# Optimization experiments

Hardware: AMD Instinct MI355X
Metric: run time of the kernel (lower is better)

## Reference

```python
import jax, jax.numpy as jnp
import numpy as np

MIN_K = 1024  # hard-negative mining floor per image (per_image=True branch)


def setup_inputs() -> dict:
    key = jax.random.key(0)
    k1, k2 = jax.random.split(key)
    B, C, D, H, W = 4, 3, 64, 256, 256
    inp = jax.random.normal(k1, (B, C, D, H, W), dtype=jnp.float32)
    tgt = jax.random.randint(k2, (B, D, H, W), 0, C, dtype=jnp.int64)
    return {"input": inp, "target": tgt}


def reference(input, target):
    b = input.shape[0]
    # per-pixel cross-entropy: -log_softmax over class dim, gathered at target
    logp = jax.nn.log_softmax(input, axis=1)                      # [B,C,D,H,W]
    ce = -jnp.take_along_axis(logp, target[:, None].astype(jnp.int32), axis=1)[:, 0]
    loss = ce.reshape(b, -1)                                      # [B, N]
    tflat = target.reshape(b, -1)                                 # [B, N]
    N = loss.shape[1]

    fg = tflat > 0                                                # [B, N]
    fg_num = fg.sum(axis=1)                                       # [B] int
    bg_num = N - fg_num                                           # [B] int
    k = jnp.minimum(bg_num, jnp.maximum(fg_num, MIN_K))           # [B] int

    # foreground term: mean of fg losses (0 if no fg)
    fg_sum = jnp.where(fg, loss, 0.0).sum(axis=1)                 # [B]
    fg_term = jnp.where(fg_num > 0,
                        fg_sum / jnp.maximum(fg_num, 1).astype(loss.dtype), 0.0)

    # background term: mean of top-k hardest bg losses (data-dependent k, fixed shapes)
    bg_masked = jnp.where(fg, -jnp.inf, loss)                     # fg -> -inf, never selected
    sorted_desc = -jnp.sort(-bg_masked, axis=1)                   # [B, N] descending
    sel = jnp.arange(N)[None, :] < k[:, None]                     # first k entries
    bg_sum = jnp.where(sel, sorted_desc, 0.0).sum(axis=1)         # [B]
    bg_term = jnp.where(bg_num > 0,
                        bg_sum / jnp.maximum(k, 1).astype(loss.dtype), 0.0)

    return jnp.sum(fg_term + bg_term) / b
```

## Files before the change

### kernel.cpp

```cpp
#include <hip/hip_runtime.h>

#define NPIX 4194304
#define BATCH 4
#define MINK 1024ULL
#define NBINS 4096
#define G1 512
#define HG 256

typedef unsigned long long u64;
typedef int vint4 __attribute__((ext_vector_type(4)));
typedef float vflt4 __attribute__((ext_vector_type(4)));

__device__ __forceinline__ float pix_loss(float v0, float v1, float v2, int t) {
    float m = fmaxf(fmaxf(v0, v1), v2);
    float lse = m + __logf(__expf(v0 - m) + __expf(v1 - m) + __expf(v2 - m));
    float xt = (t == 0) ? v0 : ((t == 1) ? v1 : v2);
    return lse - xt;
}

__global__ __launch_bounds__(256) void k_reduce(const float* __restrict__ x,
                                                const int* __restrict__ tg,
                                                float* __restrict__ pfs,
                                                float* __restrict__ pbs,
                                                unsigned* __restrict__ pfc,
                                                uint4* __restrict__ histz,
                                                unsigned* __restrict__ flags,
                                                int have_hist) {
    const int b = blockIdx.y;
    if (b == 0 && blockIdx.x < 32) {
        if (have_hist) histz[blockIdx.x * 256 + threadIdx.x] = make_uint4(0u, 0u, 0u, 0u);
        if (blockIdx.x == 0 && threadIdx.x == 0) flags[1] = 0u;
    }
    const float* xb = x + (size_t)b * 3 * NPIX;
    const int* tb = tg + (size_t)b * NPIX;
    float fs = 0.f, bs = 0.f;
    int fc = 0;
    const int stride = G1 * 256 * 4;
#pragma unroll
    for (int it = 0; it < NPIX / stride; ++it) {
        const int i = it * stride + (blockIdx.x * 256 + threadIdx.x) * 4;
        const vflt4 a = __builtin_nontemporal_load((const vflt4*)(xb + i));
        const vflt4 c = __builtin_nontemporal_load((const vflt4*)(xb + NPIX + i));
        const vflt4 d = __builtin_nontemporal_load((const vflt4*)(xb + 2 * NPIX + i));
        const vint4 t4 = __builtin_nontemporal_load((const vint4*)(tb + i));
        float l;
        l = pix_loss(a[0], c[0], d[0], t4[0]); if (t4[0] > 0) { fs += l; fc++; } else bs += l;
        l = pix_loss(a[1], c[1], d[1], t4[1]); if (t4[1] > 0) { fs += l; fc++; } else bs += l;
        l = pix_loss(a[2], c[2], d[2], t4[2]); if (t4[2] > 0) { fs += l; fc++; } else bs += l;
        l = pix_loss(a[3], c[3], d[3], t4[3]); if (t4[3] > 0) { fs += l; fc++; } else bs += l;
    }
#pragma unroll
    for (int off = 32; off > 0; off >>= 1) {
        fs += __shfl_down(fs, off);
        bs += __shfl_down(bs, off);
        fc += __shfl_down(fc, off);
    }
    __shared__ float sfs[4], sbs[4];
    __shared__ int sfc[4];
    const int wid = threadIdx.x >> 6;
    if ((threadIdx.x & 63) == 0) { sfs[wid] = fs; sbs[wid] = bs; sfc[wid] = fc; }
    __syncthreads();
    if (threadIdx.x == 0) {
        const int slot = b * G1 + blockIdx.x;
        pfs[slot] = sfs[0] + sfs[1] + sfs[2] + sfs[3];
        pbs[slot] = sbs[0] + sbs[1] + sbs[2] + sbs[3];
        pfc[slot] = (unsigned)(sfc[0] + sfc[1] + sfc[2] + sfc[3]);
    }
}

__device__ __forceinline__ void reduce_image(const float* __restrict__ pfs,
                                             const float* __restrict__ pbs,
                                             const unsigned* __restrict__ pfc,
                                             int b2, int tid,
                                             double* __restrict__ sda,
                                             double* __restrict__ sdb,
                                             unsigned* __restrict__ su,
                                             double& tfs, double& tbs, u64& tfc) {
    double fs = 0.0, bs = 0.0;
    unsigned fc = 0;
    if (tid < G1 / 4) {
        const float4 f4 = ((const float4*)pfs)[b2 * (G1 / 4) + tid];
        const float4 b4 = ((const float4*)pbs)[b2 * (G1 / 4) + tid];
        const uint4 c4 = ((const uint4*)pfc)[b2 * (G1 / 4) + tid];
        fs = (double)f4.x + (double)f4.y + (double)f4.z + (double)f4.w;
        bs = (double)b4.x + (double)b4.y + (double)b4.z + (double)b4.w;
        fc = c4.x + c4.y + c4.z + c4.w;
    }
#pragma unroll
    for (int off = 32; off > 0; off >>= 1) {
        fs += __shfl_down(fs, off);
        bs += __shfl_down(bs, off);
        fc += __shfl_down(fc, off);
    }
    const int wid = tid >> 6;
    if ((tid & 63) == 0) { sda[wid] = fs; sdb[wid] = bs; su[wid] = fc; }
    __syncthreads();
    tfs = sda[0] + sda[1] + sda[2] + sda[3];
    tbs = sdb[0] + sdb[1] + sdb[2] + sdb[3];
    tfc = (u64)su[0] + su[1] + su[2] + su[3];
    __syncthreads();
}

__global__ __launch_bounds__(256) void k_tail(const float* __restrict__ pfs,
                                              const float* __restrict__ pbs,
                                              const unsigned* __restrict__ pfc,
                                              const float* __restrict__ x,
                                              const int* __restrict__ tg,
                                              unsigned* __restrict__ hist_cnt,
                                              float* __restrict__ hist_sum,
                                              unsigned* __restrict__ flags,
                                              float* __restrict__ out,
                                              int have_hist) {
    const int b = blockIdx.y;
    const int tid = threadIdx.x;
    __shared__ double sda[4], sdb[4];
    __shared__ unsigned su[4];

    u64 fc_own;
    {
        unsigned s = 0;
        if (tid < G1 / 4) {
            const uint4 c4 = ((const uint4*)pfc)[b * (G1 / 4) + tid];
            s = c4.x + c4.y + c4.z + c4.w;
        }
#pragma unroll
        for (int off = 32; off > 0; off >>= 1) s += __shfl_down(s, off);
        if ((tid & 63) == 0) su[tid >> 6] = s;
        __syncthreads();
        fc_own = (u64)su[0] + su[1] + su[2] + su[3];
        __syncthreads();
    }
    const u64 bg_own = (u64)NPIX - fc_own;
    const u64 mk_own = fc_own > MINK ? fc_own : MINK;
    const u64 k_own = bg_own < mk_own ? bg_own : mk_own;
    const bool need_own = (k_own < bg_own) && have_hist;

    if (blockIdx.x == 0 && b == 0) {
        double acc = 0.0;
        bool any_need = false;
        for (int b2 = 0; b2 < BATCH; ++b2) {
            double tfs, tbs; u64 tfc;
            reduce_image(pfs, pbs, pfc, b2, tid, sda, sdb, su, tfs, tbs, tfc);
            const u64 bg = (u64)NPIX - tfc;
            const u64 mk = tfc > MINK ? tfc : MINK;
            const u64 k = bg < mk ? bg : mk;
            if (k < bg && have_hist) any_need = true;
            const double fg_term = (tfc > 0) ? tfs / (double)tfc : 0.0;
            const u64 kd = k > 1 ? k : 1;
            const double bg_term = (bg > 0) ? tbs / (double)kd : 0.0;
            acc += fg_term + bg_term;
        }
        if (tid == 0 && !any_need) out[0] = (float)(acc / (double)BATCH);
    }

    if (!need_own) return;

    __shared__ unsigned hc[NBINS];
    __shared__ float hs[NBINS];
    for (int i = tid; i < NBINS; i += 256) { hc[i] = 0u; hs[i] = 0.f; }
    __syncthreads();
    {
        const float* xb = x + (size_t)b * 3 * NPIX;
        const int* tb = tg + (size_t)b * NPIX;
        const int stride = HG * 256 * 4;
        for (int i = (blockIdx.x * 256 + tid) * 4; i < NPIX; i += stride) {
            const float4 a = *(const float4*)(xb + i);
            const float4 c = *(const float4*)(xb + NPIX + i);
            const float4 d = *(const float4*)(xb + 2 * NPIX + i);
            const int4 t4 = *(const int4*)(tb + i);
            float v[4][3] = {{a.x, c.x, d.x}, {a.y, c.y, d.y}, {a.z, c.z, d.z}, {a.w, c.w, d.w}};
            int tt[4] = {t4.x, t4.y, t4.z, t4.w};
#pragma unroll
            for (int j = 0; j < 4; ++j) {
                if (tt[j] == 0) {
                    float l = fmaxf(pix_loss(v[j][0], v[j][1], v[j][2], tt[j]), 0.f);
                    unsigned bin = __float_as_uint(l) >> 20;
                    atomicAdd(&hc[bin], 1u);
                    atomicAdd(&hs[bin], l);
                }
            }
        }
    }
    __syncthreads();
    for (int i = tid; i < NBINS; i += 256) {
        if (hc[i]) {
            atomicAdd(&hist_cnt[(size_t)b * NBINS + i], hc[i]);
            atomicAdd(&hist_sum[(size_t)b * NBINS + i], hs[i]);
        }
    }

    int nneed = 0;
    for (int b2 = 0; b2 < BATCH; ++b2) {
        unsigned s = 0;
        if (tid < G1 / 4) {
            const uint4 c4 = ((const uint4*)pfc)[b2 * (G1 / 4) + tid];
            s = c4.x + c4.y + c4.z + c4.w;
        }
#pragma unroll
        for (int off = 32; off > 0; off >>= 1) s += __shfl_down(s, off);
        if ((tid & 63) == 0) su[tid >> 6] = s;
        __syncthreads();
        const u64 fc2 = (u64)su[0] + su[1] + su[2] + su[3];
        __syncthreads();
        const u64 bg2 = (u64)NPIX - fc2;
        const u64 mk2 = fc2 > MINK ? fc2 : MINK;
        const u64 k2 = bg2 < mk2 ? bg2 : mk2;
        if (k2 < bg2) nneed++;
    }

    __threadfence();
    __syncthreads();
    __shared__ int is_last;
    if (tid == 0) {
        unsigned v = atomicAdd(&flags[1], 1u);
        is_last = (v == (unsigned)(HG * nneed) - 1u) ? 1 : 0;
    }
    __syncthreads();
    if (!is_last) return;
    __threadfence();

    double acc = 0.0;
    for (int b2 = 0; b2 < BATCH; ++b2) {
        double tfs, tbs; u64 tfc;
        reduce_image(pfs, pbs, pfc, b2, tid, sda, sdb, su, tfs, tbs, tfc);
        const u64 bg = (u64)NPIX - tfc;
        const u64 mk = tfc > MINK ? tfc : MINK;
        const u64 k = bg < mk ? bg : mk;
        double bg_sel = tbs;
        if (k < bg) {
            for (int i = tid; i < NBINS; i += 256) {
                hc[i] = __hip_atomic_load(&hist_cnt[(size_t)b2 * NBINS + i],
                                          __ATOMIC_ACQUIRE, __HIP_MEMORY_SCOPE_AGENT);
                hs[i] = __hip_atomic_load(&hist_sum[(size_t)b2 * NBINS + i],
                                          __ATOMIC_ACQUIRE, __HIP_MEMORY_SCOPE_AGENT);
            }
            __syncthreads();
            if (tid == 0) {
                u64 cnt = 0; double s = 0.0, topk = 0.0;
                for (int i = NBINS - 1; i >= 0; --i) {
                    unsigned c = hc[i];
                    if (cnt + c >= k) {
                        double edge = (double)__uint_as_float(((unsigned)i) << 20);
                        topk = s + (double)(k - cnt) * edge;
                        break;
                    }
                    cnt += c;
                    s += (double)hs[i];
                }
                sda[0] = topk;
            }
            __syncthreads();
            bg_sel = sda[0];
            __syncthreads();
        }
        const double fg_term = (tfc > 0) ? tfs / (double)tfc : 0.0;
        const u64 kd = k > 1 ? k : 1;
        const double bg_term = (bg > 0) ? bg_sel / (double)kd : 0.0;
        acc += fg_term + bg_term;
    }
    if (tid == 0) out[0] = (float)(acc / (double)BATCH);
}

extern "C" void kernel_launch(void* const* d_in, const int* in_sizes, int n_in,
                              void* d_out, int out_size, void* d_ws, size_t ws_size,
                              hipStream_t stream) {
    const float* x = (const float*)d_in[0];
    const int* tg = (const int*)d_in[1];
    float* out = (float*)d_out;

    char* ws = (char*)d_ws;
    float* pfs = (float*)ws;
    float* pbs = (float*)(ws + 16384);
    unsigned* pfc = (unsigned*)(ws + 32768);
    unsigned* flags = (unsigned*)(ws + 49152);
    unsigned* hist_cnt = (unsigned*)(ws + 49280);
    float* hist_sum = (float*)(ws + 49280 + (size_t)BATCH * NBINS * 4);
    uint4* histz = (uint4*)(ws + 49280);
    const size_t need_ws = 49280 + (size_t)BATCH * NBINS * 8;
    const int have_hist = (ws_size >= need_ws) ? 1 : 0;

    dim3 block(256);
    dim3 grid1(G1, BATCH);
    k_reduce<<<grid1, block, 0, stream>>>(x, tg, pfs, pbs, pfc, histz, flags, have_hist);
    dim3 grid2(HG, BATCH);
    k_tail<<<grid2, block, 0, stream>>>(pfs, pbs, pfc, x, tg,
                                        hist_cnt, hist_sum, flags, out, have_hist);
}
```

Before: 50.81 us.

## Finalize loss in last reduce block and early-exit tail kernel via need mask

The reduce kernel now uses a last-block atomic counter to compute the final loss and a per-image mask of which images need top-k histogram selection. It writes the mask to flags[0]. The tail kernel reads this mask and exits at once when no image needs selection, so its blocks no longer each redo the partial-count reduction. The reduce loop also processes two strided iterations per step to put more loads in flight. The counter is never reset; the modulo check on it relies on the total block count being a power of two.

```diff
diff --git a/kernel.cpp b/kernel.cpp
--- a/kernel.cpp
+++ b/kernel.cpp
@@ -5,6 +5,7 @@
 #define MINK 1024ULL
 #define NBINS 4096
 #define G1 512
+#define TOT (G1 * BATCH)
 #define HG 256
 
 typedef unsigned long long u64;
@@ -16,56 +17,6 @@
     float lse = m + __logf(__expf(v0 - m) + __expf(v1 - m) + __expf(v2 - m));
     float xt = (t == 0) ? v0 : ((t == 1) ? v1 : v2);
     return lse - xt;
-}
-
-__global__ __launch_bounds__(256) void k_reduce(const float* __restrict__ x,
-                                                const int* __restrict__ tg,
-                                                float* __restrict__ pfs,
-                                                float* __restrict__ pbs,
-                                                unsigned* __restrict__ pfc,
-                                                uint4* __restrict__ histz,
-                                                unsigned* __restrict__ flags,
-                                                int have_hist) {
-    const int b = blockIdx.y;
-    if (b == 0 && blockIdx.x < 32) {
-        if (have_hist) histz[blockIdx.x * 256 + threadIdx.x] = make_uint4(0u, 0u, 0u, 0u);
-        if (blockIdx.x == 0 && threadIdx.x == 0) flags[1] = 0u;
-    }
-    const float* xb = x + (size_t)b * 3 * NPIX;
-    const int* tb = tg + (size_t)b * NPIX;
-    float fs = 0.f, bs = 0.f;
-    int fc = 0;
-    const int stride = G1 * 256 * 4;
-#pragma unroll
-    for (int it = 0; it < NPIX / stride; ++it) {
-        const int i = it * stride + (blockIdx.x * 256 + threadIdx.x) * 4;
-        const vflt4 a = __builtin_nontemporal_load((const vflt4*)(xb + i));
-        const vflt4 c = __builtin_nontemporal_load((const vflt4*)(xb + NPIX + i));
-        const vflt4 d = __builtin_nontemporal_load((const vflt4*)(xb + 2 * NPIX + i));
-        const vint4 t4 = __builtin_nontemporal_load((const vint4*)(tb + i));
-        float l;
-        l = pix_loss(a[0], c[0], d[0], t4[0]); if (t4[0] > 0) { fs += l; fc++; } else bs += l;
-        l = pix_loss(a[1], c[1], d[1], t4[1]); if (t4[1] > 0) { fs += l; fc++; } else bs += l;
-        l = pix_loss(a[2], c[2], d[2], t4[2]); if (t4[2] > 0) { fs += l; fc++; } else bs += l;
-        l = pix_loss(a[3], c[3], d[3], t4[3]); if (t4[3] > 0) { fs += l; fc++; } else bs += l;
-    }
-#pragma unroll
-    for (int off = 32; off > 0; off >>= 1) {
-        fs += __shfl_down(fs, off);
-        bs += __shfl_down(bs, off);
-        fc += __shfl_down(fc, off);
-    }
-    __shared__ float sfs[4], sbs[4];
-    __shared__ int sfc[4];
-    const int wid = threadIdx.x >> 6;
-    if ((threadIdx.x & 63) == 0) { sfs[wid] = fs; sbs[wid] = bs; sfc[wid] = fc; }
-    __syncthreads();
-    if (threadIdx.x == 0) {
-        const int slot = b * G1 + blockIdx.x;
-        pfs[slot] = sfs[0] + sfs[1] + sfs[2] + sfs[3];
-        pbs[slot] = sbs[0] + sbs[1] + sbs[2] + sbs[3];
-        pfc[slot] = (unsigned)(sfc[0] + sfc[1] + sfc[2] + sfc[3]);
-    }
 }
 
 __device__ __forceinline__ void reduce_image(const float* __restrict__ pfs,
@@ -101,6 +52,97 @@
     __syncthreads();
 }
 
+__global__ __launch_bounds__(256) void k_reduce(const float* __restrict__ x,
+                                                const int* __restrict__ tg,
+                                                float* __restrict__ pfs,
+                                                float* __restrict__ pbs,
+                                                unsigned* __restrict__ pfc,
+                                                uint4* __restrict__ histz,
+                                                unsigned* __restrict__ flags,
+                                                float* __restrict__ out,
+                                                int have_hist) {
+    const int b = blockIdx.y;
+    if (b == 0 && blockIdx.x < 32) {
+        if (have_hist) histz[blockIdx.x * 256 + threadIdx.x] = make_uint4(0u, 0u, 0u, 0u);
+        if (blockIdx.x == 0 && threadIdx.x == 0) flags[1] = 0u;
+    }
+    const float* xb = x + (size_t)b * 3 * NPIX;
+    const int* tb = tg + (size_t)b * NPIX;
+    float fs = 0.f, bs = 0.f;
+    int fc = 0;
+    const int base = (blockIdx.x * 256 + threadIdx.x) * 4;
+    const int stride = G1 * 256 * 4;
+#pragma unroll
+    for (int it = 0; it < NPIX / stride; it += 2) {
+        const int i0 = it * stride + base;
+        const int i1 = i0 + stride;
+        const vflt4 a0 = __builtin_nontemporal_load((const vflt4*)(xb + i0));
+        const vflt4 c0 = __builtin_nontemporal_load((const vflt4*)(xb + NPIX + i0));
+        const vflt4 d0 = __builtin_nontemporal_load((const vflt4*)(xb + 2 * NPIX + i0));
+        const vint4 t0 = __builtin_nontemporal_load((const vint4*)(tb + i0));
+        const vflt4 a1 = __builtin_nontemporal_load((const vflt4*)(xb + i1));
+        const vflt4 c1 = __builtin_nontemporal_load((const vflt4*)(xb + NPIX + i1));
+        const vflt4 d1 = __builtin_nontemporal_load((const vflt4*)(xb + 2 * NPIX + i1));
+        const vint4 t1 = __builtin_nontemporal_load((const vint4*)(tb + i1));
+        float l;
+#pragma unroll
+        for (int j = 0; j < 4; ++j) {
+            l = pix_loss(a0[j], c0[j], d0[j], t0[j]);
+            if (t0[j] > 0) { fs += l; fc++; } else bs += l;
+        }
+#pragma unroll
+        for (int j = 0; j < 4; ++j) {
+            l = pix_loss(a1[j], c1[j], d1[j], t1[j]);
+            if (t1[j] > 0) { fs += l; fc++; } else bs += l;
+        }
+    }
+#pragma unroll
+    for (int off = 32; off > 0; off >>= 1) {
+        fs += __shfl_down(fs, off);
+        bs += __shfl_down(bs, off);
+        fc += __shfl_down(fc, off);
+    }
+    __shared__ float sfs[4], sbs[4];
+    __shared__ int sfc[4];
+    const int wid = threadIdx.x >> 6;
+    if ((threadIdx.x & 63) == 0) { sfs[wid] = fs; sbs[wid] = bs; sfc[wid] = fc; }
+    __syncthreads();
+    __shared__ int lastf;
+    if (threadIdx.x == 0) {
+        const int slot = b * G1 + blockIdx.x;
+        pfs[slot] = sfs[0] + sfs[1] + sfs[2] + sfs[3];
+        pbs[slot] = sbs[0] + sbs[1] + sbs[2] + sbs[3];
+        pfc[slot] = (unsigned)(sfc[0] + sfc[1] + sfc[2] + sfc[3]);
+        __threadfence();
+        unsigned old = atomicAdd(&flags[16], 1u);
+        lastf = ((old & (unsigned)(TOT - 1)) == (unsigned)(TOT - 1)) ? 1 : 0;
+    }
+    __syncthreads();
+    if (!lastf) return;
+    __threadfence();
+
+    __shared__ double sda[4], sdb[4];
+    __shared__ unsigned su[4];
+    double acc = 0.0;
+    unsigned mask = 0u;
+    for (int b2 = 0; b2 < BATCH; ++b2) {
+        double tfs, tbs; u64 tfc;
+        reduce_image(pfs, pbs, pfc, b2, threadIdx.x, sda, sdb, su, tfs, tbs, tfc);
+        const u64 bg = (u64)NPIX - tfc;
+        const u64 mk = tfc > MINK ? tfc : MINK;
+        const u64 k = bg < mk ? bg : mk;
+        if (k < bg && have_hist) mask |= (1u << b2);
+        const double fg_term = (tfc > 0) ? tfs / (double)tfc : 0.0;
+        const u64 kd = k > 1 ? k : 1;
+        const double bg_term = (bg > 0) ? tbs / (double)kd : 0.0;
+        acc += fg_term + bg_term;
+    }
+    if (threadIdx.x == 0) {
+        flags[0] = mask;
+        if (mask == 0u) out[0] = (float)(acc / (double)BATCH);
+    }
+}
+
 __global__ __launch_bounds__(256) void k_tail(const float* __restrict__ pfs,
                                               const float* __restrict__ pbs,
                                               const unsigned* __restrict__ pfc,
@@ -109,51 +151,12 @@
                                               unsigned* __restrict__ hist_cnt,
                                               float* __restrict__ hist_sum,
                                               unsigned* __restrict__ flags,
-                                              float* __restrict__ out,
-                                              int have_hist) {
+                                              float* __restrict__ out) {
+    const unsigned need = flags[0];
+    if (need == 0u) return;
     const int b = blockIdx.y;
     const int tid = threadIdx.x;
-    __shared__ double sda[4], sdb[4];
-    __shared__ unsigned su[4];
-
-    u64 fc_own;
-    {
-        unsigned s = 0;
-        if (tid < G1 / 4) {
-            const uint4 c4 = ((const uint4*)pfc)[b * (G1 / 4) + tid];
-            s = c4.x + c4.y + c4.z + c4.w;
-        }
-#pragma unroll
-        for (int off = 32; off > 0; off >>= 1) s += __shfl_down(s, off);
-        if ((tid & 63) == 0) su[tid >> 6] = s;
-        __syncthreads();
-        fc_own = (u64)su[0] + su[1] + su[2] + su[3];
-        __syncthreads();
-    }
-    const u64 bg_own = (u64)NPIX - fc_own;
-    const u64 mk_own = fc_own > MINK ? fc_own : MINK;
-    const u64 k_own = bg_own < mk_own ? bg_own : mk_own;
-    const bool need_own = (k_own < bg_own) && have_hist;
-
-    if (blockIdx.x == 0 && b == 0) {
-        double acc = 0.0;
-        bool any_need = false;
-        for (int b2 = 0; b2 < BATCH; ++b2) {
-            double tfs, tbs; u64 tfc;
-            reduce_image(pfs, pbs, pfc, b2, tid, sda, sdb, su, tfs, tbs, tfc);
-            const u64 bg = (u64)NPIX - tfc;
-            const u64 mk = tfc > MINK ? tfc : MINK;
-            const u64 k = bg < mk ? bg : mk;
-            if (k < bg && have_hist) any_need = true;
-            const double fg_term = (tfc > 0) ? tfs / (double)tfc : 0.0;
-            const u64 kd = k > 1 ? k : 1;
-            const double bg_term = (bg > 0) ? tbs / (double)kd : 0.0;
-            acc += fg_term + bg_term;
-        }
-        if (tid == 0 && !any_need) out[0] = (float)(acc / (double)BATCH);
-    }
-
-    if (!need_own) return;
+    if (!(need & (1u << b))) return;
 
     __shared__ unsigned hc[NBINS];
     __shared__ float hs[NBINS];
@@ -189,25 +192,7 @@
         }
     }
 
-    int nneed = 0;
-    for (int b2 = 0; b2 < BATCH; ++b2) {
-        unsigned s = 0;
-        if (tid < G1 / 4) {
-            const uint4 c4 = ((const uint4*)pfc)[b2 * (G1 / 4) + tid];
-            s = c4.x + c4.y + c4.z + c4.w;
-        }
-#pragma unroll
-        for (int off = 32; off > 0; off >>= 1) s += __shfl_down(s, off);
-        if ((tid & 63) == 0) su[tid >> 6] = s;
-        __syncthreads();
-        const u64 fc2 = (u64)su[0] + su[1] + su[2] + su[3];
-        __syncthreads();
-        const u64 bg2 = (u64)NPIX - fc2;
-        const u64 mk2 = fc2 > MINK ? fc2 : MINK;
-        const u64 k2 = bg2 < mk2 ? bg2 : mk2;
-        if (k2 < bg2) nneed++;
-    }
-
+    const int nneed = __popc(need);
     __threadfence();
     __syncthreads();
     __shared__ int is_last;
@@ -219,6 +204,8 @@
     if (!is_last) return;
     __threadfence();
 
+    __shared__ double sda[4], sdb[4];
+    __shared__ unsigned su[4];
     double acc = 0.0;
     for (int b2 = 0; b2 < BATCH; ++b2) {
         double tfs, tbs; u64 tfc;
@@ -227,7 +214,7 @@
         const u64 mk = tfc > MINK ? tfc : MINK;
         const u64 k = bg < mk ? bg : mk;
         double bg_sel = tbs;
-        if (k < bg) {
+        if (need & (1u << b2)) {
             for (int i = tid; i < NBINS; i += 256) {
                 hc[i] = __hip_atomic_load(&hist_cnt[(size_t)b2 * NBINS + i],
                                           __ATOMIC_ACQUIRE, __HIP_MEMORY_SCOPE_AGENT);
@@ -281,8 +268,10 @@
 
     dim3 block(256);
     dim3 grid1(G1, BATCH);
-    k_reduce<<<grid1, block, 0, stream>>>(x, tg, pfs, pbs, pfc, histz, flags, have_hist);
-    dim3 grid2(HG, BATCH);
-    k_tail<<<grid2, block, 0, stream>>>(pfs, pbs, pfc, x, tg,
-                                        hist_cnt, hist_sum, flags, out, have_hist);
-}
+    k_reduce<<<grid1, block, 0, stream>>>(x, tg, pfs, pbs, pfc, histz, flags, out, have_hist);
+    if (have_hist) {
+        dim3 grid2(HG, BATCH);
+        k_tail<<<grid2, block, 0, stream>>>(pfs, pbs, pfc, x, tg,
+                                            hist_cnt, hist_sum, flags, out);
+    }
+}
```

After: 145.7 us. +186.7%, slower.
